# Optimization experiments

Measured on AMD Instinct MI355X. Metric: run time of the kernel, lower is better.

## Reference

```python
import jax, jax.numpy as jnp
import numpy as np

A_BITS = 16
W_BITS = 8
KH = KW = 3
STRIDE = 1
PADDING = 1


def fake_quant(x, bits, axes=None):
    """Asymmetric min/max fake quantization with straight-through estimator."""
    if axes is None:
        mn = x.min()
        mx = x.max()
    else:
        mn = x.min(axis=axes, keepdims=True)
        mx = x.max(axis=axes, keepdims=True)
    qmax = float(2 ** bits - 1)
    scale = jnp.maximum((mx - mn) / qmax, 1e-12)
    zp = jnp.round(-mn / scale)
    q = jnp.clip(jnp.round(x / scale) + zp, 0.0, qmax)
    deq = (q - zp) * scale
    # STE: identity gradient through the quantizer
    return x + jax.lax.stop_gradient(deq - x)


def unfold(x, kh, kw, stride, padding):
    """torch.nn.functional.unfold equivalent -> (N, C*kh*kw, Hout*Wout)."""
    N, C, H, W = x.shape
    xp = jnp.pad(x, ((0, 0), (0, 0), (padding, padding), (padding, padding)))
    Ho = (H - kh + 2 * padding) // stride + 1
    Wo = (W - kw + 2 * padding) // stride + 1
    cols = []
    for i in range(kh):          # small fixed 3x3 loop
        for j in range(kw):
            cols.append(xp[:, :, i:i + Ho * stride:stride, j:j + Wo * stride:stride])
    xcol = jnp.stack(cols, axis=2)              # (N, C, kh*kw, Ho, Wo)
    return xcol.reshape(N, C * kh * kw, Ho * Wo), Ho, Wo


def adder_op(W_col, X_col):
    # W_col: (F, K), X_col: (K, L) -> out: (F, L); L1-distance "conv"
    return -jnp.abs(W_col[:, :, None] - X_col[None, :, :]).sum(axis=1)


def setup_inputs() -> dict:
    key = jax.random.key(0)
    kx, kw = jax.random.split(key)
    x = jax.random.normal(kx, (4, 64, 28, 28), dtype=jnp.float32)
    W = jax.random.normal(kw, (64, 64, 3, 3), dtype=jnp.float32)
    return {"x": x, "W": W}


def reference(x, W):
    # first_layer == 0 -> activation fake-quant; per-channel weight fake-quant
    qx = fake_quant(x, A_BITS)
    qw = fake_quant(W, W_BITS, axes=(1, 2, 3))
    N = x.shape[0]
    F = W.shape[0]
    xcol, Ho, Wo = unfold(qx, KH, KW, STRIDE, PADDING)   # (N, K, L0)
    K = xcol.shape[1]
    # torch: permute(1,2,0).view(K, L0*N) -> batch fastest within a row
    X_col = jnp.transpose(xcol, (1, 2, 0)).reshape(K, -1)  # (K, L0*N)
    W_col = qw.reshape(F, K)
    out = adder_op(W_col, X_col)                            # (F, L0*N)
    out = out.reshape(F, Ho, Wo, N).transpose(3, 0, 1, 2)   # (N, F, Ho, Wo)
    return out
```

## Files before the change

### kernel.cpp

```cpp
#include <hip/hip_runtime.h>
#include <math.h>

#define N_  4
#define C_  64
#define H_  28
#define W_  28
#define F_  64
#define KK  576
#define NX  (N_*C_*H_*W_)
#define NX4 (NX/4)


__global__ __launch_bounds__(256) void k_prep(const float* __restrict__ x,
                                              const float* __restrict__ Wg,
                                              float* __restrict__ ws) {
  __shared__ float sm[4], sM[4];
  int tid = threadIdx.x, lane = tid & 63, wv = tid >> 6;

  const float4* x4 = (const float4*)x;
  float m = 3.4e38f, M = -3.4e38f;
  for (int i = blockIdx.x * 256 + tid; i < NX4; i += 64 * 256) {
    float4 v = x4[i];
    m = fminf(m, fminf(fminf(v.x, v.y), fminf(v.z, v.w)));
    M = fmaxf(M, fmaxf(fmaxf(v.x, v.y), fmaxf(v.z, v.w)));
  }
  #pragma unroll
  for (int o = 32; o; o >>= 1) {
    m = fminf(m, __shfl_xor(m, o));
    M = fmaxf(M, __shfl_xor(M, o));
  }
  if (lane == 0) { sm[wv] = m; sM[wv] = M; }
  __syncthreads();
  if (tid == 0) {
    m = fminf(fminf(sm[0], sm[1]), fminf(sm[2], sm[3]));
    M = fmaxf(fmaxf(sM[0], sM[1]), fmaxf(sM[2], sM[3]));
    ws[blockIdx.x] = m;
    ws[64 + blockIdx.x] = M;
  }

  if (blockIdx.x < 16) {
    int f = blockIdx.x * 4 + wv;
    const float* wp = Wg + f * KK;
    float v[9];
    float wm = 3.4e38f, wM = -3.4e38f;
    #pragma unroll
    for (int u = 0; u < 9; ++u) {
      v[u] = wp[lane + 64 * u];
      wm = fminf(wm, v[u]);
      wM = fmaxf(wM, v[u]);
    }
    #pragma unroll
    for (int o = 32; o; o >>= 1) {
      wm = fminf(wm, __shfl_xor(wm, o));
      wM = fmaxf(wM, __shfl_xor(wM, o));
    }
    float s = fmaxf((wM - wm) / 255.0f, 1e-12f);
    float z = rintf(-wm / s);
    float rs = 1.0f / s;
    float* Wt = ws + 256;
    #pragma unroll
    for (int u = 0; u < 9; ++u) {
      float q = fminf(fmaxf(rintf(v[u] * rs) + z, 0.0f), 255.0f);
      Wt[(lane + 64 * u) * 64 + f] = (q - z) * s;
    }
  }
}

__global__ __launch_bounds__(256, 1) void k_main(const float* __restrict__ x,
                                                 const float* __restrict__ ws,
                                                 float* __restrict__ out) {
  __shared__ __align__(16) float Xs[64 * 3 * 32];
  __shared__ float Rbuf[8 * 32 * 29];
  int tid = threadIdx.x;
  int lane = tid & 63;
  int fl = tid & 31, cq = tid >> 5;
  int y = blockIdx.x, n = blockIdx.y, fh = blockIdx.z;

  float m = ws[lane], M = ws[64 + lane];
  #pragma unroll
  for (int o = 32; o; o >>= 1) {
    m = fminf(m, __shfl_xor(m, o));
    M = fmaxf(M, __shfl_xor(M, o));
  }
  float sx = fmaxf((M - m) / 65535.0f, 1e-12f);
  float zx = rintf(-m / sx);
  float rx = 1.0f / sx;

  for (int idx = tid; idx < 64 * 3 * 30; idx += 256) {
    int c = idx / 90, rem = idx - c * 90;
    int r = rem / 30, p = rem - r * 30;
    int row = y + r - 1, col = p - 1;
    float v = 0.0f;
    if ((unsigned)row < 28u && (unsigned)col < 28u) {
      float raw = x[((n * 64 + c) * 28 + row) * 28 + col];
      float q = fminf(fmaxf(rintf(raw * rx) + zx, 0.0f), 65535.0f);
      v = (q - zx) * sx;
    }
    Xs[(c * 3 + r) * 32 + p] = v;
  }
  __syncthreads();

  const float* Wt = ws + 256;
  int f = fh * 32 + fl;
  float acc[28];
  #pragma unroll
  for (int i = 0; i < 28; ++i) acc[i] = 0.0f;

  float w[9], wn[9];
  {
    const float* wp = Wt + (cq * 8) * 9 * 64 + f;
    #pragma unroll
    for (int k = 0; k < 9; ++k) wn[k] = wp[k * 64];
  }
  for (int ci = 0; ci < 8; ++ci) {
    #pragma unroll
    for (int k = 0; k < 9; ++k) w[k] = wn[k];
    if (ci < 7) {
      const float* wp = Wt + (cq * 8 + ci + 1) * 9 * 64 + f;
      #pragma unroll
      for (int k = 0; k < 9; ++k) wn[k] = wp[k * 64];
    }
    const float* xr = &Xs[(cq * 8 + ci) * 96];
    #pragma unroll
    for (int p = 0; p < 28; ++p) {
      float s0 = fabsf(w[0] - xr[p])      + fabsf(w[1] - xr[p + 1])  + fabsf(w[2] - xr[p + 2]);
      float s1 = fabsf(w[3] - xr[32 + p]) + fabsf(w[4] - xr[33 + p]) + fabsf(w[5] - xr[34 + p]);
      float s2 = fabsf(w[6] - xr[64 + p]) + fabsf(w[7] - xr[65 + p]) + fabsf(w[8] - xr[66 + p]);
      acc[p] += s0 + s1 + s2;
    }
  }

  #pragma unroll
  for (int p = 0; p < 28; ++p) Rbuf[(cq * 32 + fl) * 29 + p] = acc[p];
  __syncthreads();

  for (int i = 0; i < 4; ++i) {
    int idx = tid + 256 * i;
    if (idx < 896) {
      int ff = idx / 28, col = idx - ff * 28;
      float s = 0.0f;
      #pragma unroll
      for (int q = 0; q < 8; ++q) s += Rbuf[(q * 32 + ff) * 29 + col];
      out[((n * 64 + fh * 32 + ff) * 28 + y) * 28 + col] = -s;
    }
  }
}

extern "C" void kernel_launch(void* const* d_in, const int* in_sizes, int n_in,
                              void* d_out, int out_size, void* d_ws, size_t ws_size,
                              hipStream_t stream) {
  const float* x  = (const float*)d_in[0];
  const float* Wg = (const float*)d_in[1];
  float* out = (float*)d_out;
  float* ws  = (float*)d_ws;

  hipLaunchKernelGGL(k_prep, dim3(64), dim3(256), 0, stream, x, Wg, ws);
  hipLaunchKernelGGL(k_main, dim3(28, 4, 2), dim3(256), 0, stream, x, ws, out);
}
```

Before: 82.50 us.

## Register-block two filters per thread and vectorize shared-memory row loads

Each thread now computes two output filters (f and f+16) instead of one, so each loaded input value is reused across two weight sets. Input rows are pulled from shared memory as float4 into a register array, and the channel stride is padded to 100. Channels are split 16 ways instead of 8, which doubles the final reduction buffer and its summation loop. The point is to cut LDS traffic per FLOP. The cost is higher register pressure from 56 accumulators plus a 32-float row buffer, which could cause spills.

```diff
diff --git a/kernel.cpp b/kernel.cpp
--- a/kernel.cpp
+++ b/kernel.cpp
@@ -9,6 +9,8 @@
 #define KK  576
 #define NX  (N_*C_*H_*W_)
 #define NX4 (NX/4)
+
+#define CH_STRIDE 100
 
 
 __global__ __launch_bounds__(256) void k_prep(const float* __restrict__ x,
@@ -69,11 +71,11 @@
 __global__ __launch_bounds__(256, 1) void k_main(const float* __restrict__ x,
                                                  const float* __restrict__ ws,
                                                  float* __restrict__ out) {
-  __shared__ __align__(16) float Xs[64 * 3 * 32];
-  __shared__ float Rbuf[8 * 32 * 29];
+  __shared__ __align__(16) float Xs[64 * CH_STRIDE];
+  __shared__ float Rbuf[16 * 32 * 29];
   int tid = threadIdx.x;
   int lane = tid & 63;
-  int fl = tid & 31, cq = tid >> 5;
+  int fl = tid & 15, cq = tid >> 4;
   int y = blockIdx.x, n = blockIdx.y, fh = blockIdx.z;
 
   float m = ws[lane], M = ws[64 + lane];
@@ -96,51 +98,64 @@
       float q = fminf(fmaxf(rintf(raw * rx) + zx, 0.0f), 65535.0f);
       v = (q - zx) * sx;
     }
-    Xs[(c * 3 + r) * 32 + p] = v;
+    Xs[c * CH_STRIDE + r * 32 + p] = v;
   }
   __syncthreads();
 
   const float* Wt = ws + 256;
-  int f = fh * 32 + fl;
-  float acc[28];
+  int f0 = fh * 32 + fl;
+  float acc0[28], acc1[28];
   #pragma unroll
-  for (int i = 0; i < 28; ++i) acc[i] = 0.0f;
+  for (int i = 0; i < 28; ++i) { acc0[i] = 0.0f; acc1[i] = 0.0f; }
 
-  float w[9], wn[9];
+  float wc[18], wn[18];
   {
-    const float* wp = Wt + (cq * 8) * 9 * 64 + f;
+    const float* wp = Wt + (cq * 9) * 64 + f0;
     #pragma unroll
-    for (int k = 0; k < 9; ++k) wn[k] = wp[k * 64];
+    for (int k = 0; k < 9; ++k) { wn[k] = wp[k * 64]; wn[9 + k] = wp[k * 64 + 16]; }
   }
-  for (int ci = 0; ci < 8; ++ci) {
+
+  for (int ci = 0; ci < 4; ++ci) {
     #pragma unroll
-    for (int k = 0; k < 9; ++k) w[k] = wn[k];
-    if (ci < 7) {
-      const float* wp = Wt + (cq * 8 + ci + 1) * 9 * 64 + f;
+    for (int k = 0; k < 18; ++k) wc[k] = wn[k];
+    if (ci < 3) {
+      int cn = cq + 16 * (ci + 1);
+      const float* wp = Wt + (cn * 9) * 64 + f0;
       #pragma unroll
-      for (int k = 0; k < 9; ++k) wn[k] = wp[k * 64];
+      for (int k = 0; k < 9; ++k) { wn[k] = wp[k * 64]; wn[9 + k] = wp[k * 64 + 16]; }
     }
-    const float* xr = &Xs[(cq * 8 + ci) * 96];
+    int c = cq + 16 * ci;
     #pragma unroll
-    for (int p = 0; p < 28; ++p) {
-      float s0 = fabsf(w[0] - xr[p])      + fabsf(w[1] - xr[p + 1])  + fabsf(w[2] - xr[p + 2]);
-      float s1 = fabsf(w[3] - xr[32 + p]) + fabsf(w[4] - xr[33 + p]) + fabsf(w[5] - xr[34 + p]);
-      float s2 = fabsf(w[6] - xr[64 + p]) + fabsf(w[7] - xr[65 + p]) + fabsf(w[8] - xr[66 + p]);
-      acc[p] += s0 + s1 + s2;
+    for (int r = 0; r < 3; ++r) {
+      const float4* xr4 = (const float4*)&Xs[c * CH_STRIDE + r * 32];
+      float xv[32];
+      #pragma unroll
+      for (int i = 0; i < 8; ++i) ((float4*)xv)[i] = xr4[i];
+      float wa0 = wc[3 * r], wa1 = wc[3 * r + 1], wa2 = wc[3 * r + 2];
+      float wb0 = wc[9 + 3 * r], wb1 = wc[9 + 3 * r + 1], wb2 = wc[9 + 3 * r + 2];
+      #pragma unroll
+      for (int p = 0; p < 28; ++p) {
+        acc0[p] += fabsf(wa0 - xv[p]) + fabsf(wa1 - xv[p + 1]) + fabsf(wa2 - xv[p + 2]);
+        acc1[p] += fabsf(wb0 - xv[p]) + fabsf(wb1 - xv[p + 1]) + fabsf(wb2 - xv[p + 2]);
+      }
     }
   }
 
   #pragma unroll
-  for (int p = 0; p < 28; ++p) Rbuf[(cq * 32 + fl) * 29 + p] = acc[p];
+  for (int p = 0; p < 28; ++p) {
+    Rbuf[(cq * 32 + fl) * 29 + p] = acc0[p];
+    Rbuf[(cq * 32 + fl + 16) * 29 + p] = acc1[p];
+  }
   __syncthreads();
 
+  #pragma unroll
   for (int i = 0; i < 4; ++i) {
     int idx = tid + 256 * i;
     if (idx < 896) {
       int ff = idx / 28, col = idx - ff * 28;
       float s = 0.0f;
       #pragma unroll
-      for (int q = 0; q < 8; ++q) s += Rbuf[(q * 32 + ff) * 29 + col];
+      for (int q = 0; q < 16; ++q) s += Rbuf[(q * 32 + ff) * 29 + col];
       out[((n * 64 + fh * 32 + ff) * 28 + y) * 28 + col] = -s;
     }
   }
```

Result: faster. 80.58 us (-2.3%).
